# Kernel optimization log

Hardware: AMD Instinct MI355X
Metric: run time of the kernel (lower is better)

Reference implementation:

```python
import jax, jax.numpy as jnp
import numpy as np

B, D, H, W = 16, 256, 32, 32
K = 4096
LIM = 3 ** 0.5  # codebook init range from the module


def setup_inputs() -> dict:
    key = jax.random.key(0)
    kx, kc = jax.random.split(key)
    x = jax.random.normal(kx, (B, D, H, W), dtype=jnp.float32)
    codebook = jax.random.uniform(kc, (K, D), dtype=jnp.float32) * LIM
    return {"x": x, "codebook": codebook}


def reference(x, codebook):
    # x: [B, D, H, W] -> flat tokens [B*H*W, D]
    b, d, h, w = x.shape
    flat = jnp.transpose(x, (0, 2, 3, 1)).reshape(-1, d)
    # Squared Euclidean distances (argmin identical to cdist p=2 argmin):
    # ||a||^2 - 2 a.b + ||b||^2
    d2 = (
        jnp.sum(flat * flat, axis=-1, keepdims=True)
        - 2.0 * flat @ codebook.T
        + jnp.sum(codebook * codebook, axis=-1)
    )  # [N, K]
    idx = jnp.argmin(d2, axis=1)  # [N]
    quantized = codebook[idx]  # gather, [N, D]
    quantized = quantized.reshape(b, h, w, d)
    return jnp.transpose(quantized, (0, 3, 1, 2))  # [B, D, H, W]
```

## Files before the change

kernel.cpp:

```cpp
#include <hip/hip_runtime.h>
#include <math.h>

#define DD    256
#define HWD   1024
#define NTOK  16384
#define KK    4096

typedef __attribute__((ext_vector_type(8))) short     bf16x8;
typedef __attribute__((ext_vector_type(4))) float     f32x4;
typedef __attribute__((ext_vector_type(8))) unsigned short ushort8;

__device__ __forceinline__ unsigned short f2bf(float f) {
    unsigned u = __float_as_uint(f);
    unsigned r = (u + 0x7FFFu + ((u >> 16) & 1u)) >> 16;
    return (unsigned short)r;
}
__device__ __forceinline__ float bf2f(unsigned short h) {
    return __uint_as_float(((unsigned)h) << 16);
}

#define GLOAD16(gaddr, laddr)                                                   \
    __builtin_amdgcn_global_load_lds(                                           \
        (const __attribute__((address_space(1))) unsigned int*)(gaddr),         \
        (__attribute__((address_space(3))) unsigned int*)(laddr), 16, 0, 0)

__global__ __launch_bounds__(256) void vq_splitx(const float* __restrict__ x,
                                                 unsigned short* __restrict__ Ax) {
    const int blk = blockIdx.x;
    const int tid = threadIdx.x;
    const int b = blk >> 4;
    const int hw0 = (blk & 15) << 6;

    __shared__ float xls[DD * 64];

    const float* xb = x + (size_t)b * (DD * HWD) + hw0;
    #pragma unroll 8
    for (int it = 0; it < 64; ++it) {
        int e = it * 256 + tid;
        int d = e >> 6, i = e & 63;
        xls[d * 64 + i] = xb[d * HWD + i];
    }
    __syncthreads();

    const int tok_l = tid >> 2;
    const int part  = tid & 3;
    const int n = b * HWD + hw0 + tok_l;
    unsigned short* dst = Ax + (size_t)n * 768 + part * 192;

    #pragma unroll
    for (int c8 = 0; c8 < 8; ++c8) {
        const int dbase = part * 64 + c8 * 8;
        ushort8 w0, w1, w2;
        #pragma unroll
        for (int q = 0; q < 8; ++q) {
            float v = xls[(dbase + q) * 64 + tok_l];
            unsigned short hq = f2bf(v);
            unsigned short lq = f2bf(v - bf2f(hq));
            const int i0 = 3 * q, i1 = 3 * q + 1, i2 = 3 * q + 2;
            if (i0 < 8) w0[i0] = hq; else if (i0 < 16) w1[i0 - 8] = hq; else w2[i0 - 16] = hq;
            if (i1 < 8) w0[i1] = lq; else if (i1 < 16) w1[i1 - 8] = lq; else w2[i1 - 16] = lq;
            if (i2 < 8) w0[i2] = hq; else if (i2 < 16) w1[i2 - 8] = hq; else w2[i2 - 16] = hq;
        }
        *(ushort8*)(dst + c8 * 24)      = w0;
        *(ushort8*)(dst + c8 * 24 + 8)  = w1;
        *(ushort8*)(dst + c8 * 24 + 16) = w2;
    }
}

__global__ __launch_bounds__(256) void vq_splitc(const float* __restrict__ cb,
                                                 unsigned short* __restrict__ Bc) {
    const int gid = blockIdx.x * 256 + threadIdx.x;
    const int k = gid >> 5;
    const int j = gid & 31;
    const float4* cb4 = (const float4*)cb;
    float4 a = cb4[k * 64 + j * 2];
    float4 bq = cb4[k * 64 + j * 2 + 1];
    float vv[8] = {a.x, a.y, a.z, a.w, bq.x, bq.y, bq.z, bq.w};
    ushort8 w0, w1, w2;
    #pragma unroll
    for (int q = 0; q < 8; ++q) {
        unsigned short hq = f2bf(vv[q]);
        unsigned short lq = f2bf(vv[q] - bf2f(hq));
        const int i0 = 3 * q, i1 = 3 * q + 1, i2 = 3 * q + 2;
        if (i0 < 8) w0[i0] = hq; else if (i0 < 16) w1[i0 - 8] = hq; else w2[i0 - 16] = hq;
        if (i1 < 8) w0[i1] = hq; else if (i1 < 16) w1[i1 - 8] = hq; else w2[i1 - 16] = hq;
        if (i2 < 8) w0[i2] = lq; else if (i2 < 16) w1[i2 - 8] = lq; else w2[i2 - 16] = lq;
    }
    unsigned short* dst = Bc + (size_t)k * 768 + j * 24;
    *(ushort8*)(dst)      = w0;
    *(ushort8*)(dst + 8)  = w1;
    *(ushort8*)(dst + 16) = w2;
}

__global__ __launch_bounds__(256) void vq_transpose(const float* __restrict__ cb,
                                                    float* __restrict__ cbT) {
    __shared__ float t[32][33];
    const int kt = blockIdx.x * 32, dt = blockIdx.y * 32;
    const int tx = threadIdx.x & 31, ty = threadIdx.x >> 5;
    #pragma unroll
    for (int r = 0; r < 32; r += 8)
        t[ty + r][tx] = cb[(kt + ty + r) * DD + dt + tx];
    __syncthreads();
    #pragma unroll
    for (int r = 0; r < 32; r += 8)
        cbT[(size_t)(dt + ty + r) * KK + kt + tx] = t[tx][ty + r];
}

__global__ __launch_bounds__(256) void vq_cnorm(const float* __restrict__ cb,
                                                float* __restrict__ cnorm) {
    int k = (blockIdx.x * 256 + threadIdx.x) >> 6;
    int lane = threadIdx.x & 63;
    float4 v = reinterpret_cast<const float4*>(cb)[k * 64 + lane];
    float s = v.x * v.x + v.y * v.y + v.z * v.z + v.w * v.w;
    #pragma unroll
    for (int off = 32; off > 0; off >>= 1) s += __shfl_xor(s, off, 64);
    if (lane == 0) cnorm[k] = s;
}

__global__ void vq_zero(int* cnt) { if (threadIdx.x == 0) *cnt = 0; }

#define BM 128
#define BN 128
#define BK 64
#define KRED 768
#define NPH 4
#define NT_PER_PH 8
#define MARGIN 0.05f

__global__ __launch_bounds__(256, 2) void vq_gemm_min(
    const unsigned short* __restrict__ Ax,
    const unsigned short* __restrict__ Bc,
    const float* __restrict__ cnorm,
    float* __restrict__ candb, float* __restrict__ cands, int* __restrict__ candk)
{
    const int tid  = threadIdx.x;
    const int wid  = tid >> 6, lane = tid & 63;
    const int wm   = wid >> 1, wn = wid & 1;
    const int l15  = lane & 15, l4 = lane >> 4;
    const int mblk = blockIdx.x;
    const int phase = blockIdx.y;

    __shared__ alignas(16) unsigned short As[BM * BK];
    __shared__ alignas(16) unsigned short Bs[BN * BK];
    __shared__ float mrg[BM][2][3];

    float runb[16], runs[16];
    int   runk[16];
    #pragma unroll
    for (int e = 0; e < 16; ++e) { runb[e] = 3.0e38f; runs[e] = 3.0e38f; runk[e] = 0; }

    const int stage_row = (lane >> 3);
    const int stage_c16 = (lane & 7);

    for (int nt = 0; nt < NT_PER_PH; ++nt) {
        f32x4 acc[4][4];
        #pragma unroll
        for (int mi = 0; mi < 4; ++mi)
            #pragma unroll
            for (int ni = 0; ni < 4; ++ni)
                acc[mi][ni] = (f32x4){0.f, 0.f, 0.f, 0.f};

        for (int kk = 0; kk < KRED / BK; ++kk) {
            __syncthreads();
            #pragma unroll
            for (int ib = 0; ib < 4; ++ib) {
                const int rb = wid * 32 + ib * 8;
                const int ldsoff = __builtin_amdgcn_readfirstlane(rb * 64);
                const int rA = rb + stage_row;
                GLOAD16(Ax + (size_t)(mblk * BM + rA) * KRED + kk * BK + stage_c16 * 8,
                        &As[ldsoff]);
                GLOAD16(Bc + (size_t)(phase * 1024 + nt * BN + rA) * KRED + kk * BK + stage_c16 * 8,
                        &Bs[ldsoff]);
            }
            __syncthreads();

            #pragma unroll
            for (int kh = 0; kh < 2; ++kh) {
                bf16x8 af[4], bfr[4];
                #pragma unroll
                for (int mi = 0; mi < 4; ++mi) {
                    int r = wm * 64 + mi * 16 + l15;
                    af[mi] = *(const bf16x8*)&As[r * BK + kh * 32 + l4 * 8];
                }
                #pragma unroll
                for (int ni = 0; ni < 4; ++ni) {
                    int c = wn * 64 + ni * 16 + l15;
                    bfr[ni] = *(const bf16x8*)&Bs[c * BK + kh * 32 + l4 * 8];
                }
                #pragma unroll
                for (int mi = 0; mi < 4; ++mi)
                    #pragma unroll
                    for (int ni = 0; ni < 4; ++ni)
                        acc[mi][ni] = __builtin_amdgcn_mfma_f32_16x16x32_bf16(
                            af[mi], bfr[ni], acc[mi][ni], 0, 0, 0);
            }
        }

        #pragma unroll
        for (int ni = 0; ni < 4; ++ni) {
            const int c = phase * 1024 + nt * BN + wn * 64 + ni * 16 + l15;
            const float cn = cnorm[c];
            #pragma unroll
            for (int mi = 0; mi < 4; ++mi) {
                #pragma unroll
                for (int rg = 0; rg < 4; ++rg) {
                    float d = fmaf(-2.0f, acc[mi][ni][rg], cn);
                    const int e = mi * 4 + rg;
                    float ob = runb[e];
                    runs[e] = fminf(fmaxf(d, ob), runs[e]);
                    runk[e] = (d < ob) ? c : runk[e];
                    runb[e] = fminf(d, ob);
                }
            }
        }
    }

    #pragma unroll
    for (int e = 0; e < 16; ++e) {
        float b = runb[e], s = runs[e];
        int   k = runk[e];
        #pragma unroll
        for (int off = 1; off < 16; off <<= 1) {
            float ob = __shfl_xor(b, off, 64);
            float os = __shfl_xor(s, off, 64);
            int   ok = __shfl_xor(k, off, 64);
            float nb = fminf(b, ob);
            s = fminf(fminf(s, os), fmaxf(b, ob));
            k = (ob < b) ? ok : k;
            b = nb;
        }
        if (l15 == 0) {
            int row = wm * 64 + (e >> 2) * 16 + l4 * 4 + (e & 3);
            mrg[row][wn][0] = b;
            mrg[row][wn][1] = s;
            mrg[row][wn][2] = __int_as_float(k);
        }
    }
    __syncthreads();

    if (tid < BM) {
        const int row = tid;
        float b0 = mrg[row][0][0], s0 = mrg[row][0][1];
        float b1 = mrg[row][1][0], s1 = mrg[row][1][1];
        int   k0 = __float_as_int(mrg[row][0][2]);
        int   k1 = __float_as_int(mrg[row][1][2]);
        float b = fminf(b0, b1);
        float s = fminf(fminf(s0, s1), fmaxf(b0, b1));
        int   k = (b1 < b0) ? k1 : k0;
        const int tok = mblk * BM + row;
        candb[phase * NTOK + tok] = b;
        cands[phase * NTOK + tok] = s;
        candk[phase * NTOK + tok] = k;
    }
}

__global__ __launch_bounds__(256) void vq_merge(
    const float* __restrict__ candb, const float* __restrict__ cands,
    const int* __restrict__ candk, int* __restrict__ out_k,
    int* __restrict__ flagged, int* __restrict__ cnt,
    unsigned long long* __restrict__ packed)
{
    const int tok = blockIdx.x * 256 + threadIdx.x;
    float b = candb[tok], s = cands[tok];
    int   k = candk[tok];
    #pragma unroll
    for (int p = 1; p < NPH; ++p) {
        float pb = candb[p * NTOK + tok], ps = cands[p * NTOK + tok];
        int   pk = candk[p * NTOK + tok];
        float nb = fminf(b, pb);
        s = fminf(fminf(s, ps), fmaxf(b, pb));
        k = (pb < b) ? pk : k;
        b = nb;
    }
    out_k[tok] = k;
    if (s - b < MARGIN) {
        int i = atomicAdd(cnt, 1);
        flagged[i] = tok;
        packed[i] = 0xFFFFFFFFFFFFFFFFull;
    }
}

__global__ __launch_bounds__(256) void vq_exact(
    const float* __restrict__ x, const float* __restrict__ cbT,
    const float* __restrict__ cnorm, const int* __restrict__ flagged,
    const int* __restrict__ cnt, unsigned long long* __restrict__ packed)
{
    const int tid = threadIdx.x;
    const int lane = tid & 63, wid = tid >> 6;
    const int items = (*cnt) << 2;
    __shared__ float xs[DD];
    __shared__ unsigned long long wbest[4];

    for (int w = blockIdx.x; w < items; w += gridDim.x) {
        const int ti = w >> 2;
        const int ch = w & 3;
        const int tok = flagged[ti];
        const int b = tok >> 10, hw = tok & 1023;
        __syncthreads();
        xs[tid] = x[(size_t)b * (DD * HWD) + tid * HWD + hw];
        __syncthreads();

        const int kbase = ch * 1024 + tid * 4;
        float a0 = 0.f, a1 = 0.f, a2 = 0.f, a3 = 0.f;
        #pragma unroll 8
        for (int d = 0; d < DD; ++d) {
            const float xv = xs[d];
            const float4 cv = *(const float4*)(cbT + (size_t)d * KK + kbase);
            a0 = fmaf(xv, cv.x, a0);
            a1 = fmaf(xv, cv.y, a1);
            a2 = fmaf(xv, cv.z, a2);
            a3 = fmaf(xv, cv.w, a3);
        }
        float d0 = fmaf(-2.f, a0, cnorm[kbase]);
        float d1 = fmaf(-2.f, a1, cnorm[kbase + 1]);
        float d2 = fmaf(-2.f, a2, cnorm[kbase + 2]);
        float d3 = fmaf(-2.f, a3, cnorm[kbase + 3]);
        float best = d0; int bk = kbase;
        if (d1 < best) { best = d1; bk = kbase + 1; }
        if (d2 < best) { best = d2; bk = kbase + 2; }
        if (d3 < best) { best = d3; bk = kbase + 3; }
        unsigned ub = __float_as_uint(best);
        ub = (ub & 0x80000000u) ? ~ub : (ub | 0x80000000u);
        unsigned long long pk = ((unsigned long long)ub << 32) | (unsigned)bk;
        #pragma unroll
        for (int off = 1; off < 64; off <<= 1) {
            unsigned long long o = __shfl_xor(pk, off, 64);
            pk = (o < pk) ? o : pk;
        }
        if (lane == 0) wbest[wid] = pk;
        __syncthreads();
        if (tid == 0) {
            unsigned long long m = wbest[0];
            #pragma unroll
            for (int i = 1; i < 4; ++i) m = (wbest[i] < m) ? wbest[i] : m;
            atomicMin(&packed[ti], m);
        }
    }
}

__global__ __launch_bounds__(256) void vq_unpack(
    const int* __restrict__ flagged, const int* __restrict__ cnt,
    const unsigned long long* __restrict__ packed, int* __restrict__ out_k)
{
    const int i = blockIdx.x * 256 + threadIdx.x;
    if (i < *cnt) out_k[flagged[i]] = (int)(packed[i] & 0xFFFFFFFFull);
}

__global__ __launch_bounds__(256) void vq_gather(const float* __restrict__ cb,
                                                 const int* __restrict__ out_k,
                                                 float* __restrict__ out) {
    const int blk = blockIdx.x;
    const int tid = threadIdx.x;
    const int b = blk >> 4;
    const int hw0 = (blk & 15) << 6;

    __shared__ int   bks[64];
    __shared__ float ts[64][65];

    if (tid < 64) bks[tid] = out_k[blk * 64 + tid];
    __syncthreads();

    const int rr = tid >> 6;
    const int j  = tid & 63;
    float* ob = out + (size_t)b * (DD * HWD) + hw0;
    #pragma unroll
    for (int c = 0; c < 4; ++c) {
        const int d0 = c << 6;
        #pragma unroll 4
        for (int it = 0; it < 16; ++it) {
            int tok = it * 4 + rr;
            ts[tok][j] = cb[bks[tok] * DD + d0 + j];
        }
        __syncthreads();
        #pragma unroll 4
        for (int it = 0; it < 16; ++it) {
            int dl = it * 4 + rr;
            ob[(d0 + dl) * HWD + j] = ts[j][dl];
        }
        __syncthreads();
    }
}

#define TT2   64
#define KGRP2 16
#define NW2   16
__global__ __launch_bounds__(1024, 8) void vq_dist2(const float* __restrict__ x,
                                                    const float* __restrict__ cbT,
                                                    const float* __restrict__ cnorm,
                                                    float* __restrict__ cand_d,
                                                    int* __restrict__ cand_k) {
    const int blk = blockIdx.x;
    const int phase = blockIdx.y;
    const int tid = threadIdx.x;
    const int wid = tid >> 6, lane = tid & 63;
    const int b = blk >> 4;
    const int hw0 = (blk & 15) << 6;

    __shared__ alignas(16) float xs[DD * TT2];
    __shared__ float bd_s[NW2][TT2];
    __shared__ int   bk_s[NW2][TT2];

    const float* xb = x + (size_t)b * (DD * HWD) + hw0;
    #pragma unroll
    for (int it = 0; it < 16; ++it) {
        int e = it * 1024 + tid;
        int d = e >> 6, i = e & 63;
        xs[(d >> 1) * 128 + i * 2 + (d & 1)] = xb[d * HWD + i];
    }
    __syncthreads();

    const float2* xs2 = reinterpret_cast<const float2*>(xs) + lane;
    float best = 3.0e38f;
    int bestk = 0;
    const int g0 = phase * 128 + wid * 8;
    for (int j = 0; j < 8; ++j) {
        const int k0 = __builtin_amdgcn_readfirstlane((g0 + j) * KGRP2);
        const float* __restrict__ cT0 = cbT + k0;
        const float* __restrict__ cn0 = cnorm + k0;
        float acc[KGRP2];
        #pragma unroll
        for (int t = 0; t < KGRP2; ++t) acc[t] = 0.f;
        #pragma unroll 4
        for (int d2 = 0; d2 < DD / 2; ++d2) {
            float2 xv = xs2[d2 * 64];
            const float* __restrict__ cA = cT0 + (size_t)(2 * d2) * KK;
            const float* __restrict__ cB = cA + KK;
            #pragma unroll
            for (int t = 0; t < KGRP2; ++t) acc[t] = fmaf(xv.x, cA[t], acc[t]);
            #pragma unroll
            for (int t = 0; t < KGRP2; ++t) acc[t] = fmaf(xv.y, cB[t], acc[t]);
        }
        #pragma unroll
        for (int t = 0; t < KGRP2; ++t) {
            float dv = fmaf(-2.0f, acc[t], cn0[t]);
            if (dv < best) { best = dv; bestk = k0 + t; }
        }
    }
    bd_s[wid][lane] = best;
    bk_s[wid][lane] = bestk;
    __syncthreads();
    if (tid < TT2) {
        float bdv = bd_s[0][lane];
        int   bkv = bk_s[0][lane];
        #pragma unroll
        for (int w = 1; w < NW2; ++w) {
            float ddv = bd_s[w][lane];
            int   kw = bk_s[w][lane];
            if (ddv < bdv || (ddv == bdv && kw < bkv)) { bdv = ddv; bkv = kw; }
        }
        int nn = blk * TT2 + lane;
        cand_d[phase * NTOK + nn] = bdv;
        cand_k[phase * NTOK + nn] = bkv;
    }
}

__global__ __launch_bounds__(256) void vq_merge2(const float* __restrict__ cand_d,
                                                 const int* __restrict__ cand_k,
                                                 int* __restrict__ out_k) {
    const int tok = blockIdx.x * 256 + threadIdx.x;
    float d0 = cand_d[tok]; int k0 = cand_k[tok];
    float d1 = cand_d[NTOK + tok]; int k1 = cand_k[NTOK + tok];
    out_k[tok] = (d1 < d0 || (d1 == d0 && k1 < k0)) ? k1 : k0;
}

extern "C" void kernel_launch(void* const* d_in, const int* in_sizes, int n_in,
                              void* d_out, int out_size, void* d_ws, size_t ws_size,
                              hipStream_t stream) {
    const float* x  = (const float*)d_in[0];
    const float* cb = (const float*)d_in[1];
    float* out = (float*)d_out;

    char* w = (char*)d_ws;
    float* cbT    = (float*)(w);
    float* cnorm  = (float*)(w + 4194304);
    int*   out_k  = (int*)  (w + 4210688);
    int*   cnt    = (int*)  (w + 4276224);
    int*   flagged= (int*)  (w + 4276480);
    float* candb  = (float*)(w + 4342016);
    float* cands  = (float*)(w + 4604160);
    int*   candk  = (int*)  (w + 4866304);
    unsigned long long* packed = (unsigned long long*)(w + 5128448);
    unsigned short* Ax = (unsigned short*)(w + 5259520);
    unsigned short* Bc = (unsigned short*)(w + 30425344);
    const size_t BIG_NEED = 36716800;

    vq_transpose<<<dim3(KK / 32, DD / 32), dim3(256), 0, stream>>>(cb, cbT);
    vq_cnorm<<<dim3(KK / 4), dim3(256), 0, stream>>>(cb, cnorm);

    if (ws_size >= BIG_NEED) {
        vq_splitx<<<dim3(256), dim3(256), 0, stream>>>(x, Ax);
        vq_splitc<<<dim3(512), dim3(256), 0, stream>>>(cb, Bc);
        vq_zero<<<dim3(1), dim3(64), 0, stream>>>(cnt);
        vq_gemm_min<<<dim3(NTOK / BM, NPH), dim3(256), 0, stream>>>(
            Ax, Bc, cnorm, candb, cands, candk);
        vq_merge<<<dim3(NTOK / 256), dim3(256), 0, stream>>>(
            candb, cands, candk, out_k, flagged, cnt, packed);
        vq_exact<<<dim3(1024), dim3(256), 0, stream>>>(
            x, cbT, cnorm, flagged, cnt, packed);
        vq_unpack<<<dim3(NTOK / 256), dim3(256), 0, stream>>>(
            flagged, cnt, packed, out_k);
    } else {
        float* cand_d = candb;
        int*   cand_k = candk;
        vq_dist2<<<dim3(NTOK / TT2, 2), dim3(1024), 0, stream>>>(
            x, cbT, cnorm, cand_d, cand_k);
        vq_merge2<<<dim3(NTOK / 256), dim3(256), 0, stream>>>(cand_d, cand_k, out_k);
    }
    vq_gather<<<dim3(NTOK / 64), dim3(256), 0, stream>>>(cb, out_k, out);
}
```

Baseline: 280.9 us.

## Restructure VQ GEMM-min with double-buffered swizzled codebook tiles and register-direct A loads

The distance GEMM kernel now uses 64-token blocks and splits the codebook into 8 phases instead of 4, with higher occupancy (4 blocks per CU). Codebook tiles are double-buffered in LDS with an XOR swizzle, so the next tile loads while the current one computes and LDS bank conflicts drop. Token activations are read straight from global memory into registers, and the MFMA section runs at raised wave priority. In exchange the candidate buffers double in size, the merge pass has more phases to reduce, and A is re-read from global or cache per k-step.

```diff
diff --git a/kernel.cpp b/kernel.cpp
--- a/kernel.cpp
+++ b/kernel.cpp
@@ -119,15 +119,28 @@
 
 __global__ void vq_zero(int* cnt) { if (threadIdx.x == 0) *cnt = 0; }
 
-#define BM 128
 #define BN 128
 #define BK 64
 #define KRED 768
-#define NPH 4
-#define NT_PER_PH 8
+#define NPH 8
 #define MARGIN 0.05f
 
-__global__ __launch_bounds__(256, 2) void vq_gemm_min(
+__device__ __forceinline__ void stage_b(const unsigned short* __restrict__ Bc,
+                                        unsigned short* BsFlat, int buf,
+                                        int phase, int nt, int kk,
+                                        int wid, int lane) {
+    const int L3 = lane >> 3;
+    const int gcol16 = (lane & 7) ^ L3;
+    #pragma unroll
+    for (int ib = 0; ib < 4; ++ib) {
+        const int rb = wid * 32 + ib * 8;
+        const int ldsoff = __builtin_amdgcn_readfirstlane((buf << 13) + rb * 64);
+        const int code = phase * 512 + nt * 128 + rb + L3;
+        GLOAD16(Bc + (size_t)code * KRED + kk * 64 + gcol16 * 8, BsFlat + ldsoff);
+    }
+}
+
+__global__ __launch_bounds__(256, 4) void vq_gemm_min(
     const unsigned short* __restrict__ Ax,
     const unsigned short* __restrict__ Bc,
     const float* __restrict__ cnorm,
@@ -140,83 +153,83 @@
     const int mblk = blockIdx.x;
     const int phase = blockIdx.y;
 
-    __shared__ alignas(16) unsigned short As[BM * BK];
-    __shared__ alignas(16) unsigned short Bs[BN * BK];
-    __shared__ float mrg[BM][2][3];
-
-    float runb[16], runs[16];
-    int   runk[16];
-    #pragma unroll
-    for (int e = 0; e < 16; ++e) { runb[e] = 3.0e38f; runs[e] = 3.0e38f; runk[e] = 0; }
-
-    const int stage_row = (lane >> 3);
-    const int stage_c16 = (lane & 7);
-
-    for (int nt = 0; nt < NT_PER_PH; ++nt) {
-        f32x4 acc[4][4];
-        #pragma unroll
-        for (int mi = 0; mi < 4; ++mi)
-            #pragma unroll
-            for (int ni = 0; ni < 4; ++ni)
-                acc[mi][ni] = (f32x4){0.f, 0.f, 0.f, 0.f};
-
-        for (int kk = 0; kk < KRED / BK; ++kk) {
-            __syncthreads();
-            #pragma unroll
-            for (int ib = 0; ib < 4; ++ib) {
-                const int rb = wid * 32 + ib * 8;
-                const int ldsoff = __builtin_amdgcn_readfirstlane(rb * 64);
-                const int rA = rb + stage_row;
-                GLOAD16(Ax + (size_t)(mblk * BM + rA) * KRED + kk * BK + stage_c16 * 8,
-                        &As[ldsoff]);
-                GLOAD16(Bc + (size_t)(phase * 1024 + nt * BN + rA) * KRED + kk * BK + stage_c16 * 8,
-                        &Bs[ldsoff]);
+    __shared__ alignas(16) unsigned short Bs[2 * BN * BK];
+    __shared__ float mrg[64][2][3];
+
+    float runb[8], runs[8];
+    int   runk[8];
+    #pragma unroll
+    for (int e = 0; e < 8; ++e) { runb[e] = 3.0e38f; runs[e] = 3.0e38f; runk[e] = 0; }
+
+    const unsigned short* Aw =
+        Ax + (size_t)(mblk * 64 + wm * 32 + l15) * KRED + l4 * 8;
+
+    f32x4 acc[2][4];
+    #pragma unroll
+    for (int mi = 0; mi < 2; ++mi)
+        #pragma unroll
+        for (int ni = 0; ni < 4; ++ni)
+            acc[mi][ni] = (f32x4){0.f, 0.f, 0.f, 0.f};
+
+    stage_b(Bc, Bs, 0, phase, 0, 0, wid, lane);
+    __syncthreads();
+
+    int cur = 0;
+    for (int t = 0; t < 48; ++t) {
+        const int nt = t / 12, kk = t - nt * 12;
+        if (t < 47) {
+            const int t1 = t + 1;
+            const int nt1 = t1 / 12, kk1 = t1 - nt1 * 12;
+            stage_b(Bc, Bs, cur ^ 1, phase, nt1, kk1, wid, lane);
+        }
+        __builtin_amdgcn_s_setprio(1);
+        #pragma unroll
+        for (int kh = 0; kh < 2; ++kh) {
+            bf16x8 af[2], bfr[4];
+            #pragma unroll
+            for (int mi = 0; mi < 2; ++mi)
+                af[mi] = *(const bf16x8*)(Aw + (size_t)mi * 16 * KRED + kk * 64 + kh * 32);
+            #pragma unroll
+            for (int ni = 0; ni < 4; ++ni) {
+                const int r = wn * 64 + ni * 16 + l15;
+                const int c16p = ((kh * 4 + l4) ^ (l15 & 7)) * 8;
+                bfr[ni] = *(const bf16x8*)&Bs[(cur << 13) + r * 64 + c16p];
             }
-            __syncthreads();
-
-            #pragma unroll
-            for (int kh = 0; kh < 2; ++kh) {
-                bf16x8 af[4], bfr[4];
+            #pragma unroll
+            for (int mi = 0; mi < 2; ++mi)
                 #pragma unroll
-                for (int mi = 0; mi < 4; ++mi) {
-                    int r = wm * 64 + mi * 16 + l15;
-                    af[mi] = *(const bf16x8*)&As[r * BK + kh * 32 + l4 * 8];
-                }
+                for (int ni = 0; ni < 4; ++ni)
+                    acc[mi][ni] = __builtin_amdgcn_mfma_f32_16x16x32_bf16(
+                        af[mi], bfr[ni], acc[mi][ni], 0, 0, 0);
+        }
+        __builtin_amdgcn_s_setprio(0);
+
+        if (kk == 11) {
+            #pragma unroll
+            for (int ni = 0; ni < 4; ++ni) {
+                const int c = phase * 512 + nt * BN + wn * 64 + ni * 16 + l15;
+                const float cn = cnorm[c];
                 #pragma unroll
-                for (int ni = 0; ni < 4; ++ni) {
-                    int c = wn * 64 + ni * 16 + l15;
-                    bfr[ni] = *(const bf16x8*)&Bs[c * BK + kh * 32 + l4 * 8];
-                }
-                #pragma unroll
-                for (int mi = 0; mi < 4; ++mi)
+                for (int mi = 0; mi < 2; ++mi) {
                     #pragma unroll
-                    for (int ni = 0; ni < 4; ++ni)
-                        acc[mi][ni] = __builtin_amdgcn_mfma_f32_16x16x32_bf16(
-                            af[mi], bfr[ni], acc[mi][ni], 0, 0, 0);
-            }
-        }
-
-        #pragma unroll
-        for (int ni = 0; ni < 4; ++ni) {
-            const int c = phase * 1024 + nt * BN + wn * 64 + ni * 16 + l15;
-            const float cn = cnorm[c];
-            #pragma unroll
-            for (int mi = 0; mi < 4; ++mi) {
-                #pragma unroll
-                for (int rg = 0; rg < 4; ++rg) {
-                    float d = fmaf(-2.0f, acc[mi][ni][rg], cn);
-                    const int e = mi * 4 + rg;
-                    float ob = runb[e];
-                    runs[e] = fminf(fmaxf(d, ob), runs[e]);
-                    runk[e] = (d < ob) ? c : runk[e];
-                    runb[e] = fminf(d, ob);
+                    for (int rg = 0; rg < 4; ++rg) {
+                        float d = fmaf(-2.0f, acc[mi][ni][rg], cn);
+                        const int e = mi * 4 + rg;
+                        float ob = runb[e];
+                        runs[e] = fminf(fmaxf(d, ob), runs[e]);
+                        runk[e] = (d < ob) ? c : runk[e];
+                        runb[e] = fminf(d, ob);
+                    }
+                    acc[mi][ni] = (f32x4){0.f, 0.f, 0.f, 0.f};
                 }
             }
         }
-    }
-
-    #pragma unroll
-    for (int e = 0; e < 16; ++e) {
+        __syncthreads();
+        cur ^= 1;
+    }
+
+    #pragma unroll
+    for (int e = 0; e < 8; ++e) {
         float b = runb[e], s = runs[e];
         int   k = runk[e];
         #pragma unroll
@@ -230,7 +243,7 @@
             b = nb;
         }
         if (l15 == 0) {
-            int row = wm * 64 + (e >> 2) * 16 + l4 * 4 + (e & 3);
+            int row = wm * 32 + (e >> 2) * 16 + l4 * 4 + (e & 3);
             mrg[row][wn][0] = b;
             mrg[row][wn][1] = s;
             mrg[row][wn][2] = __int_as_float(k);
@@ -238,7 +251,7 @@
     }
     __syncthreads();
 
-    if (tid < BM) {
+    if (tid < 64) {
         const int row = tid;
         float b0 = mrg[row][0][0], s0 = mrg[row][0][1];
         float b1 = mrg[row][1][0], s1 = mrg[row][1][1];
@@ -247,7 +260,7 @@
         float b = fminf(b0, b1);
         float s = fminf(fminf(s0, s1), fmaxf(b0, b1));
         int   k = (b1 < b0) ? k1 : k0;
-        const int tok = mblk * BM + row;
+        const int tok = mblk * 64 + row;
         candb[phase * NTOK + tok] = b;
         cands[phase * NTOK + tok] = s;
         candk[phase * NTOK + tok] = k;
@@ -477,12 +490,12 @@
     int*   cnt    = (int*)  (w + 4276224);
     int*   flagged= (int*)  (w + 4276480);
     float* candb  = (float*)(w + 4342016);
-    float* cands  = (float*)(w + 4604160);
-    int*   candk  = (int*)  (w + 4866304);
-    unsigned long long* packed = (unsigned long long*)(w + 5128448);
-    unsigned short* Ax = (unsigned short*)(w + 5259520);
-    unsigned short* Bc = (unsigned short*)(w + 30425344);
-    const size_t BIG_NEED = 36716800;
+    float* cands  = (float*)(w + 4866304);
+    int*   candk  = (int*)  (w + 5390592);
+    unsigned long long* packed = (unsigned long long*)(w + 5914880);
+    unsigned short* Ax = (unsigned short*)(w + 6045952);
+    unsigned short* Bc = (unsigned short*)(w + 31211776);
+    const size_t BIG_NEED = 37503232;
 
     vq_transpose<<<dim3(KK / 32, DD / 32), dim3(256), 0, stream>>>(cb, cbT);
     vq_cnorm<<<dim3(KK / 4), dim3(256), 0, stream>>>(cb, cnorm);
@@ -491,7 +504,7 @@
         vq_splitx<<<dim3(256), dim3(256), 0, stream>>>(x, Ax);
         vq_splitc<<<dim3(512), dim3(256), 0, stream>>>(cb, Bc);
         vq_zero<<<dim3(1), dim3(64), 0, stream>>>(cnt);
-        vq_gemm_min<<<dim3(NTOK / BM, NPH), dim3(256), 0, stream>>>(
+        vq_gemm_min<<<dim3(NTOK / 64, NPH), dim3(256), 0, stream>>>(
             Ax, Bc, cnorm, candb, cands, candk);
         vq_merge<<<dim3(NTOK / 256), dim3(256), 0, stream>>>(
             candb, cands, candk, out_k, flagged, cnt, packed);
```

Measured after the change: 349.3 us. 1.24x slower.

## Double-buffer LDS staging in vq_gemm_min with XOR swizzle and flattened loop

Applied to the files above, without the earlier changes.

Flattens the nt/kk loops of the bf16 GEMM-argmin kernel into a single 96-step loop. The next A/B tile is prefetched into a second LDS buffer with global_load_lds while the current tile feeds the MFMAs, and explicit vmcnt waits replace the paired __syncthreads. LDS columns are XOR-swizzled to reduce bank conflicts on fragment reads, and s_setprio is raised around the MFMA block. The workspace candidate-array offsets are also shifted; the extra LDS doubles per-block shared memory, which may limit occupancy.

```diff
diff --git a/kernel.cpp b/kernel.cpp
--- a/kernel.cpp
+++ b/kernel.cpp
@@ -119,13 +119,29 @@
 
 __global__ void vq_zero(int* cnt) { if (threadIdx.x == 0) *cnt = 0; }
 
-#define BM 128
 #define BN 128
 #define BK 64
 #define KRED 768
 #define NPH 4
-#define NT_PER_PH 8
 #define MARGIN 0.05f
+
+__device__ __forceinline__ void stage_ab(const unsigned short* __restrict__ Ax,
+                                         const unsigned short* __restrict__ Bc,
+                                         unsigned short* AsF, unsigned short* BsF,
+                                         int buf, int mblk, int phase, int nt, int kk,
+                                         int wid, int lane) {
+    const int L3  = lane >> 3;
+    const int gsw = (lane & 7) ^ L3;
+    #pragma unroll
+    for (int ib = 0; ib < 4; ++ib) {
+        const int rb = wid * 32 + ib * 8;
+        const int ldsoff = __builtin_amdgcn_readfirstlane(buf * 8192 + rb * 64);
+        GLOAD16(Ax + (size_t)(mblk * 128 + rb + L3) * KRED + kk * 64 + gsw * 8,
+                AsF + ldsoff);
+        GLOAD16(Bc + (size_t)(phase * 1024 + nt * 128 + rb + L3) * KRED + kk * 64 + gsw * 8,
+                BsF + ldsoff);
+    }
+}
 
 __global__ __launch_bounds__(256, 2) void vq_gemm_min(
     const unsigned short* __restrict__ Ax,
@@ -140,79 +156,83 @@
     const int mblk = blockIdx.x;
     const int phase = blockIdx.y;
 
-    __shared__ alignas(16) unsigned short As[BM * BK];
-    __shared__ alignas(16) unsigned short Bs[BN * BK];
-    __shared__ float mrg[BM][2][3];
+    __shared__ alignas(16) unsigned short As[2 * 128 * BK];
+    __shared__ alignas(16) unsigned short Bs[2 * 128 * BK];
+    __shared__ float mrg[128][2][3];
 
     float runb[16], runs[16];
     int   runk[16];
     #pragma unroll
     for (int e = 0; e < 16; ++e) { runb[e] = 3.0e38f; runs[e] = 3.0e38f; runk[e] = 0; }
 
-    const int stage_row = (lane >> 3);
-    const int stage_c16 = (lane & 7);
-
-    for (int nt = 0; nt < NT_PER_PH; ++nt) {
-        f32x4 acc[4][4];
-        #pragma unroll
-        for (int mi = 0; mi < 4; ++mi)
-            #pragma unroll
-            for (int ni = 0; ni < 4; ++ni)
-                acc[mi][ni] = (f32x4){0.f, 0.f, 0.f, 0.f};
-
-        for (int kk = 0; kk < KRED / BK; ++kk) {
-            __syncthreads();
-            #pragma unroll
-            for (int ib = 0; ib < 4; ++ib) {
-                const int rb = wid * 32 + ib * 8;
-                const int ldsoff = __builtin_amdgcn_readfirstlane(rb * 64);
-                const int rA = rb + stage_row;
-                GLOAD16(Ax + (size_t)(mblk * BM + rA) * KRED + kk * BK + stage_c16 * 8,
-                        &As[ldsoff]);
-                GLOAD16(Bc + (size_t)(phase * 1024 + nt * BN + rA) * KRED + kk * BK + stage_c16 * 8,
-                        &Bs[ldsoff]);
+    f32x4 acc[4][4];
+    #pragma unroll
+    for (int mi = 0; mi < 4; ++mi)
+        #pragma unroll
+        for (int ni = 0; ni < 4; ++ni)
+            acc[mi][ni] = (f32x4){0.f, 0.f, 0.f, 0.f};
+
+    stage_ab(Ax, Bc, As, Bs, 0, mblk, phase, 0, 0, wid, lane);
+
+    int cur = 0;
+    for (int t = 0; t < 96; ++t) {
+        const int nt = t / 12, kk = t - nt * 12;
+        if (t < 95) {
+            const int t1 = t + 1;
+            const int nt1 = t1 / 12, kk1 = t1 - nt1 * 12;
+            stage_ab(Ax, Bc, As, Bs, cur ^ 1, mblk, phase, nt1, kk1, wid, lane);
+            asm volatile("s_waitcnt vmcnt(8)" ::: "memory");
+        } else {
+            asm volatile("s_waitcnt vmcnt(0)" ::: "memory");
+        }
+        __builtin_amdgcn_s_barrier();
+
+        __builtin_amdgcn_s_setprio(1);
+        #pragma unroll
+        for (int kh = 0; kh < 2; ++kh) {
+            bf16x8 af[4], bfr[4];
+            const int cxor = ((kh * 4 + l4) ^ (l15 & 7)) << 3;
+            #pragma unroll
+            for (int mi = 0; mi < 4; ++mi) {
+                const int r = wm * 64 + mi * 16 + l15;
+                af[mi] = *(const bf16x8*)&As[cur * 8192 + r * 64 + cxor];
             }
-            __syncthreads();
-
-            #pragma unroll
-            for (int kh = 0; kh < 2; ++kh) {
-                bf16x8 af[4], bfr[4];
+            #pragma unroll
+            for (int ni = 0; ni < 4; ++ni) {
+                const int c = wn * 64 + ni * 16 + l15;
+                bfr[ni] = *(const bf16x8*)&Bs[cur * 8192 + c * 64 + cxor];
+            }
+            #pragma unroll
+            for (int mi = 0; mi < 4; ++mi)
+                #pragma unroll
+                for (int ni = 0; ni < 4; ++ni)
+                    acc[mi][ni] = __builtin_amdgcn_mfma_f32_16x16x32_bf16(
+                        af[mi], bfr[ni], acc[mi][ni], 0, 0, 0);
+        }
+        __builtin_amdgcn_s_setprio(0);
+
+        if (kk == 11) {
+            #pragma unroll
+            for (int ni = 0; ni < 4; ++ni) {
+                const int c = phase * 1024 + nt * BN + wn * 64 + ni * 16 + l15;
+                const float cn = cnorm[c];
                 #pragma unroll
                 for (int mi = 0; mi < 4; ++mi) {
-                    int r = wm * 64 + mi * 16 + l15;
-                    af[mi] = *(const bf16x8*)&As[r * BK + kh * 32 + l4 * 8];
-                }
-                #pragma unroll
-                for (int ni = 0; ni < 4; ++ni) {
-                    int c = wn * 64 + ni * 16 + l15;
-                    bfr[ni] = *(const bf16x8*)&Bs[c * BK + kh * 32 + l4 * 8];
-                }
-                #pragma unroll
-                for (int mi = 0; mi < 4; ++mi)
                     #pragma unroll
-                    for (int ni = 0; ni < 4; ++ni)
-                        acc[mi][ni] = __builtin_amdgcn_mfma_f32_16x16x32_bf16(
-                            af[mi], bfr[ni], acc[mi][ni], 0, 0, 0);
-            }
-        }
-
-        #pragma unroll
-        for (int ni = 0; ni < 4; ++ni) {
-            const int c = phase * 1024 + nt * BN + wn * 64 + ni * 16 + l15;
-            const float cn = cnorm[c];
-            #pragma unroll
-            for (int mi = 0; mi < 4; ++mi) {
-                #pragma unroll
-                for (int rg = 0; rg < 4; ++rg) {
-                    float d = fmaf(-2.0f, acc[mi][ni][rg], cn);
-                    const int e = mi * 4 + rg;
-                    float ob = runb[e];
-                    runs[e] = fminf(fmaxf(d, ob), runs[e]);
-                    runk[e] = (d < ob) ? c : runk[e];
-                    runb[e] = fminf(d, ob);
+                    for (int rg = 0; rg < 4; ++rg) {
+                        float d = fmaf(-2.0f, acc[mi][ni][rg], cn);
+                        const int e = mi * 4 + rg;
+                        float ob = runb[e];
+                        runs[e] = fminf(fmaxf(d, ob), runs[e]);
+                        runk[e] = (d < ob) ? c : runk[e];
+                        runb[e] = fminf(d, ob);
+                    }
+                    acc[mi][ni] = (f32x4){0.f, 0.f, 0.f, 0.f};
                 }
             }
         }
+        __builtin_amdgcn_s_barrier();
+        cur ^= 1;
     }
 
     #pragma unroll
@@ -238,7 +258,7 @@
     }
     __syncthreads();
 
-    if (tid < BM) {
+    if (tid < 128) {
         const int row = tid;
         float b0 = mrg[row][0][0], s0 = mrg[row][0][1];
         float b1 = mrg[row][1][0], s1 = mrg[row][1][1];
@@ -247,7 +267,7 @@
         float b = fminf(b0, b1);
         float s = fminf(fminf(s0, s1), fmaxf(b0, b1));
         int   k = (b1 < b0) ? k1 : k0;
-        const int tok = mblk * BM + row;
+        const int tok = mblk * 128 + row;
         candb[phase * NTOK + tok] = b;
         cands[phase * NTOK + tok] = s;
         candk[phase * NTOK + tok] = k;
@@ -477,12 +497,12 @@
     int*   cnt    = (int*)  (w + 4276224);
     int*   flagged= (int*)  (w + 4276480);
     float* candb  = (float*)(w + 4342016);
-    float* cands  = (float*)(w + 4604160);
-    int*   candk  = (int*)  (w + 4866304);
-    unsigned long long* packed = (unsigned long long*)(w + 5128448);
-    unsigned short* Ax = (unsigned short*)(w + 5259520);
-    unsigned short* Bc = (unsigned short*)(w + 30425344);
-    const size_t BIG_NEED = 36716800;
+    float* cands  = (float*)(w + 4866304);
+    int*   candk  = (int*)  (w + 5390592);
+    unsigned long long* packed = (unsigned long long*)(w + 5914880);
+    unsigned short* Ax = (unsigned short*)(w + 6045952);
+    unsigned short* Bc = (unsigned short*)(w + 31211776);
+    const size_t BIG_NEED = 37503232;
 
     vq_transpose<<<dim3(KK / 32, DD / 32), dim3(256), 0, stream>>>(cb, cbT);
     vq_cnorm<<<dim3(KK / 4), dim3(256), 0, stream>>>(cb, cnorm);
@@ -491,7 +511,7 @@
         vq_splitx<<<dim3(256), dim3(256), 0, stream>>>(x, Ax);
         vq_splitc<<<dim3(512), dim3(256), 0, stream>>>(cb, Bc);
         vq_zero<<<dim3(1), dim3(64), 0, stream>>>(cnt);
-        vq_gemm_min<<<dim3(NTOK / BM, NPH), dim3(256), 0, stream>>>(
+        vq_gemm_min<<<dim3(NTOK / 128, NPH), dim3(256), 0, stream>>>(
             Ax, Bc, cnorm, candb, cands, candk);
         vq_merge<<<dim3(NTOK / 256), dim3(256), 0, stream>>>(
             candb, cands, candk, out_k, flagged, cnt, packed);
```

Measured after the change: 248.0 us. -11.7%, faster.
